# Optimization experiments

Measured on AMD Instinct MI355X. Metric: run time of the kernel, lower is better.

Reference implementation:

```python
import jax, jax.numpy as jnp
import numpy as np

N = 4096
D_IN = 512
D_H = 128
HEADS = 4
NEG_BIG = 1e10  # matches tf mask constant
LEAKY_ALPHA = 0.2  # tf.nn.leaky_relu default


def setup_inputs() -> dict:
    key = jax.random.key(0)
    ks = jax.random.split(key, 6)
    # 0/1 dense adjacency (faithful to tf.sparse.add producing dense 0/1 + mask)
    adjacency = jax.random.randint(ks[0], (N, N), 0, 2).astype(jnp.float32)
    # guarantee no empty rows (softmax over all -1e10 is degenerate)
    adjacency = adjacency.at[jnp.arange(N), jnp.arange(N)].set(1.0)
    input_feature = jax.random.normal(ks[1], (N, D_IN), dtype=jnp.float32)
    scale = 1.0 / np.sqrt(D_IN)
    kernels = jax.random.normal(ks[2], (HEADS, D_IN, D_H), dtype=jnp.float32) * scale
    biases = jnp.zeros((HEADS, D_H), dtype=jnp.float32)
    a_scale = 1.0 / np.sqrt(D_H)
    attn_self = jax.random.normal(ks[3], (HEADS, D_H), dtype=jnp.float32) * a_scale
    attn_neigh = jax.random.normal(ks[4], (HEADS, D_H), dtype=jnp.float32) * a_scale
    return {
        "adjacency": adjacency,
        "input_feature": input_feature,
        "kernels": kernels,
        "biases": biases,
        "attn_self": attn_self,
        "attn_neigh": attn_neigh,
    }


def reference(adjacency, input_feature, kernels, biases, attn_self, attn_neigh):
    # per-head feature projection: [H, N, D_h]
    feats = jnp.einsum("nd,hde->hne", input_feature, kernels)
    # additive attention logits
    a_s = jnp.einsum("hne,he->hn", feats, attn_self)   # [H, N]
    a_n = jnp.einsum("hne,he->hn", feats, attn_neigh)  # [H, N]
    dense = a_s[:, :, None] + a_n[:, None, :]          # [H, N, N]
    dense = jax.nn.leaky_relu(dense, negative_slope=LEAKY_ALPHA)
    mask = NEG_BIG * (adjacency - 1.0)                 # 0 where edge, -1e10 elsewhere
    dense = jax.nn.softmax(dense + mask[None, :, :], axis=-1)
    out = jnp.einsum("hnm,hme->hne", dense, feats) + biases[:, None, :]  # [H, N, D_h]
    # concat heads: [N, H*D_h]
    return jnp.transpose(out, (1, 0, 2)).reshape(out.shape[1], -1)
```

## Files before the change

kernel.cpp:

```cpp
#include <hip/hip_runtime.h>

#define NN 4096
#define DIN 512
#define DH 128
#define NH 4
#define L2E 1.44269504f

typedef float f32x4 __attribute__((ext_vector_type(4)));
typedef _Float16 f16x8 __attribute__((ext_vector_type(8)));
typedef _Float16 f16x4 __attribute__((ext_vector_type(4)));

__device__ __forceinline__ float leaky(float x){ return x > 0.f ? x : 0.2f*x; }

__global__ __launch_bounds__(256) void k_pack(
    const float* __restrict__ adj, unsigned int* __restrict__ bmg)
{
  int tId = blockIdx.x*256 + threadIdx.x;
  const float* p = adj + (size_t)tId*32;
  unsigned int b = 0;
  #pragma unroll
  for (int k=0;k<8;k++){
    f32x4 v = *(const f32x4*)(p + k*4);
    #pragma unroll
    for (int q=0;q<4;q++) b |= (v[q] > 0.5f) ? (1u << (k*4+q)) : 0u;
  }
  bmg[tId] = b;
}

__global__ __launch_bounds__(256) void k_gemm1(
    const float* __restrict__ X, const float* __restrict__ Kw,
    const float* __restrict__ attn_s, const float* __restrict__ attn_n,
    _Float16* __restrict__ featsT, float* __restrict__ a_s, float* __restrict__ a_n)
{
  const int it = blockIdx.x, h = blockIdx.y;
  const int i0 = it*64;
  const int t = threadIdx.x, w = t>>6, lane = t&63;
  const int eoff = (w>>1)*64, ioff = (w&1)*32;
  const int lg = lane>>4, li = lane&15;

  __shared__ _Float16 KT[128][40];
  __shared__ _Float16 XT[64][40];
  __shared__ float red_s[2][2][2][16];
  __shared__ float red_n[2][2][2][16];

  f32x4 acc[4][2] = {};

  for (int ks=0; ks<16; ++ks){
    const int d0 = ks*32;
    __syncthreads();
    #pragma unroll
    for (int q=0;q<4;q++){
      int f = t + 256*q;
      int e = f & 127, dg = (f>>7)*4;
      f16x4 hv;
      #pragma unroll
      for (int k=0;k<4;k++)
        hv[k] = (_Float16)Kw[(h*DIN + d0 + dg + k)*DH + e];
      *(f16x4*)&KT[e][dg] = hv;
    }
    #pragma unroll
    for (int q=0;q<2;q++){
      int f = t + 256*q;
      int i = f>>3, s = (f&7)*4;
      f32x4 v = *(const f32x4*)&X[(i0+i)*DIN + d0 + s];
      f16x4 hv; hv[0]=(_Float16)v[0]; hv[1]=(_Float16)v[1];
      hv[2]=(_Float16)v[2]; hv[3]=(_Float16)v[3];
      *(f16x4*)&XT[i][s] = hv;
    }
    __syncthreads();
    f16x8 af[4], bf[2];
    #pragma unroll
    for (int ef=0; ef<4; ++ef) af[ef] = *(const f16x8*)&KT[eoff + ef*16 + li][lg*8];
    #pragma unroll
    for (int f2=0; f2<2; ++f2) bf[f2] = *(const f16x8*)&XT[ioff + f2*16 + li][lg*8];
    #pragma unroll
    for (int ef=0; ef<4; ++ef)
      #pragma unroll
      for (int f2=0; f2<2; ++f2)
        acc[ef][f2] = __builtin_amdgcn_mfma_f32_16x16x32_f16(af[ef], bf[f2], acc[ef][f2], 0,0,0);
  }

  float ps[2] = {0,0}, pn[2] = {0,0};
  #pragma unroll
  for (int ef=0; ef<4; ++ef){
    #pragma unroll
    for (int r=0;r<4;r++){
      int e = eoff + ef*16 + lg*4 + r;
      float as_e = attn_s[h*DH + e];
      float an_e = attn_n[h*DH + e];
      #pragma unroll
      for (int f2=0; f2<2; ++f2){
        int irow = i0 + ioff + f2*16 + li;
        float v = acc[ef][f2][r];
        featsT[(h*DH + e)*NN + irow] = (_Float16)v;
        ps[f2] += v*as_e; pn[f2] += v*an_e;
      }
    }
  }
  #pragma unroll
  for (int f2=0; f2<2; ++f2){
    ps[f2] += __shfl_xor(ps[f2], 16); ps[f2] += __shfl_xor(ps[f2], 32);
    pn[f2] += __shfl_xor(pn[f2], 16); pn[f2] += __shfl_xor(pn[f2], 32);
  }
  if (lane < 16){
    red_s[w>>1][w&1][0][lane] = ps[0]; red_s[w>>1][w&1][1][lane] = ps[1];
    red_n[w>>1][w&1][0][lane] = pn[0]; red_n[w>>1][w&1][1][lane] = pn[1];
  }
  __syncthreads();
  if (t < 64){
    int ih = t>>5, fb = (t>>4)&1, l2 = t&15;
    a_s[h*NN + i0 + t] = red_s[0][ih][fb][l2] + red_s[1][ih][fb][l2];
    a_n[h*NN + i0 + t] = red_n[0][ih][fb][l2] + red_n[1][ih][fb][l2];
  }
}

__global__ void k_amax(const float* __restrict__ a_n, float* __restrict__ Amax,
                       float* __restrict__ EA_g, float* __restrict__ GA_g){
  int h = blockIdx.x, t = threadIdx.x;
  float m = -3.4e38f;
  for (int i=t; i<NN; i+=256){
    float v = a_n[h*NN+i];
    m = fmaxf(m, v);
    EA_g[h*NN+i] = __builtin_exp2f(v*L2E);
    GA_g[h*NN+i] = __builtin_exp2f(0.2f*v*L2E);
  }
  #pragma unroll
  for (int s=1; s<64; s<<=1) m = fmaxf(m, __shfl_xor(m, s));
  __shared__ float sm[4];
  if ((t&63)==0) sm[t>>6] = m;
  __syncthreads();
  if (t==0) Amax[h] = fmaxf(fmaxf(sm[0],sm[1]), fmaxf(sm[2],sm[3]));
}

__global__ __launch_bounds__(256, 3) void k_pv(
    const unsigned int* __restrict__ bmg, const _Float16* __restrict__ featsT,
    const float* __restrict__ a_s, const float* __restrict__ Amax,
    const float* __restrict__ EA_g, const float* __restrict__ GA_g,
    _Float16* __restrict__ Opart, float* __restrict__ Dpart)
{
  const int it = blockIdx.x, h = blockIdx.y, jcI = blockIdx.z;
  const int i0 = it*128, j0 = jcI*1024;
  const int t = threadIdx.x, w = t>>6, lane = t&63;
  const int lg = lane>>4, li = lane&15;

  __shared__ _Float16 ft[3][128*32];
  __shared__ float EA_s[1024], GA_s[1024];
  __shared__ unsigned char bm_s[128*144];

  __builtin_amdgcn_global_load_lds(
      (const __attribute__((address_space(1))) void*)(EA_g + h*NN + j0 + t*4),
      (__attribute__((address_space(3))) void*)(&EA_s[t*4]), 16, 0, 0);
  __builtin_amdgcn_global_load_lds(
      (const __attribute__((address_space(1))) void*)(GA_g + h*NN + j0 + t*4),
      (__attribute__((address_space(3))) void*)(&GA_s[t*4]), 16, 0, 0);
  #pragma unroll
  for (int p=0;p<4;p++){
    int idx = p*256 + t;
    int r = idx>>3, c = idx&7;
    uint4 v = *(const uint4*)((const char*)bmg + (size_t)(i0+r)*(NN/8) + jcI*128 + c*16);
    *(uint4*)&bm_s[r*144 + c*16] = v;
  }

  const int r0 = w*32 + li, r1 = r0 + 16;
  const float am = Amax[h];
  const float as0 = a_s[h*NN + i0 + r0];
  const float as1 = a_s[h*NN + i0 + r1];
  const float m0 = leaky(as0 + am), m1 = leaky(as1 + am);
  const float E0 = __builtin_exp2f((as0 - m0)*L2E);
  const float G0 = __builtin_exp2f((0.2f*as0 - m0)*L2E);
  const float E1 = __builtin_exp2f((as1 - m1)*L2E);
  const float G1 = __builtin_exp2f((0.2f*as1 - m1)*L2E);

  auto STAGE = [&](int buf, int js){
    #pragma unroll
    for (int q=0;q<2;q++){
      int idx = q*256 + t;
      int r = idx>>2, p = idx&3;
      int l = p ^ ((r>>1)&3);
      __builtin_amdgcn_global_load_lds(
          (const __attribute__((address_space(1))) void*)(featsT + (size_t)(h*DH + r)*NN + j0 + js*32 + l*8),
          (__attribute__((address_space(3))) void*)(&ft[buf][idx*8]), 16, 0, 0);
    }
  };

  STAGE(0, 0);
  STAGE(1, 1);
  __syncthreads();

  f32x4 acc0[8] = {}, acc1[8] = {};
  f32x4 accd0 = {}, accd1 = {};
  f16x8 ones;
  #pragma unroll
  for (int q=0;q<8;q++) ones[q] = (_Float16)1.0f;

  const int slot = lg ^ ((li>>1)&3);

  for (int js=0; js<32; ++js){
    const int cur = js % 3;
    asm volatile("s_waitcnt vmcnt(2)" ::: "memory");
    __builtin_amdgcn_s_barrier();
    {
      int nst = js+2 <= 31 ? js+2 : 31;
      STAGE((js+2) % 3, nst);
    }

    const int jb = js*32 + lg*8;
    f32x4 ea0 = *(const f32x4*)&EA_s[jb];
    f32x4 ea1 = *(const f32x4*)&EA_s[jb+4];
    f32x4 ga0 = *(const f32x4*)&GA_s[jb];
    f32x4 ga1 = *(const f32x4*)&GA_s[jb+4];
    unsigned int b0 = bm_s[r0*144 + js*4 + lg];
    unsigned int b1 = bm_s[r1*144 + js*4 + lg];

    f16x8 af0, af1;
    #pragma unroll
    for (int q=0;q<8;q++){
      float ev = (q<4) ? ea0[q] : ea1[q-4];
      float gv = (q<4) ? ga0[q] : ga1[q-4];
      float w0 = fmaxf(E0*ev, G0*gv);
      float w1 = fmaxf(E1*ev, G1*gv);
      unsigned mq0 = (unsigned)(((int)(b0 << (31-q))) >> 31);
      unsigned mq1 = (unsigned)(((int)(b1 << (31-q))) >> 31);
      w0 = __builtin_bit_cast(float, __builtin_bit_cast(unsigned, w0) & mq0);
      w1 = __builtin_bit_cast(float, __builtin_bit_cast(unsigned, w1) & mq1);
      af0[q] = (_Float16)w0;
      af1[q] = (_Float16)w1;
    }

    #pragma unroll
    for (int ef=0; ef<8; ++ef){
      f16x8 bfr = *(const f16x8*)&ft[cur][(ef*16+li)*32 + slot*8];
      acc0[ef] = __builtin_amdgcn_mfma_f32_16x16x32_f16(af0, bfr, acc0[ef], 0,0,0);
      acc1[ef] = __builtin_amdgcn_mfma_f32_16x16x32_f16(af1, bfr, acc1[ef], 0,0,0);
    }
    accd0 = __builtin_amdgcn_mfma_f32_16x16x32_f16(af0, ones, accd0, 0,0,0);
    accd1 = __builtin_amdgcn_mfma_f32_16x16x32_f16(af1, ones, accd1, 0,0,0);
  }

  const size_t chb = (size_t)(jcI*4 + h)*NN;
  if (li == 0){
    *(f32x4*)&Dpart[chb + i0 + w*32 + lg*4] = accd0;
    *(f32x4*)&Dpart[chb + i0 + w*32 + 16 + lg*4] = accd1;
  }
  #pragma unroll
  for (int ef=0; ef<8; ++ef)
    #pragma unroll
    for (int r=0;r<4;r++){
      int row0 = i0 + w*32 + lg*4 + r;
      Opart[(chb + row0)*DH + ef*16 + li] = (_Float16)acc0[ef][r];
      Opart[(chb + row0 + 16)*DH + ef*16 + li] = (_Float16)acc1[ef][r];
    }
}

__global__ __launch_bounds__(256) void k_out(
    const _Float16* __restrict__ Opart, const float* __restrict__ Dpart,
    const float* __restrict__ bias, float* __restrict__ out)
{
  int gid = blockIdx.x*256 + threadIdx.x;
  int base = gid*4;
  int i = base >> 9;
  int he = base & 511;
  int h = he >> 7;
  int e = he & 127;
  float n0=0,n1=0,n2=0,n3=0, den=0;
  #pragma unroll
  for (int jc=0; jc<4; ++jc){
    int ch = (jc*4+h)*NN + i;
    f16x4 v = *(const f16x4*)(Opart + (size_t)ch*DH + e);
    n0 += (float)v[0]; n1 += (float)v[1]; n2 += (float)v[2]; n3 += (float)v[3];
    den += Dpart[ch];
  }
  float inv = 1.f/den;
  f32x4 b4 = *(const f32x4*)&bias[he];
  f32x4 o; o[0]=n0*inv+b4[0]; o[1]=n1*inv+b4[1]; o[2]=n2*inv+b4[2]; o[3]=n3*inv+b4[3];
  *(f32x4*)&out[base] = o;
}

extern "C" void kernel_launch(void* const* d_in, const int* in_sizes, int n_in,
                              void* d_out, int out_size, void* d_ws, size_t ws_size,
                              hipStream_t stream)
{
  const float* adj   = (const float*)d_in[0];
  const float* X     = (const float*)d_in[1];
  const float* Kw    = (const float*)d_in[2];
  const float* bias  = (const float*)d_in[3];
  const float* atn_s = (const float*)d_in[4];
  const float* atn_n = (const float*)d_in[5];
  float* out = (float*)d_out;

  char* ws = (char*)d_ws;
  _Float16* featsT = (_Float16*)ws;
  unsigned int* bmg = (unsigned int*)(ws + ((size_t)4<<20));
  float* a_s  = (float*)(ws + (size_t)6*1024*1024);
  float* a_n  = a_s + NH*NN;
  float* Amax = a_n + NH*NN;
  float* EA_g = Amax + 64;
  float* GA_g = EA_g + NH*NN;
  float* Dpart = GA_g + NH*NN;
  _Float16* Opart = (_Float16*)(Dpart + 4*NH*NN);

  hipLaunchKernelGGL(k_pack, dim3(2048), dim3(256), 0, stream, adj, bmg);
  hipLaunchKernelGGL(k_gemm1, dim3(64,4), dim3(256), 0, stream,
                     X, Kw, atn_s, atn_n, featsT, a_s, a_n);
  hipLaunchKernelGGL(k_amax, dim3(4), dim3(256), 0, stream, a_n, Amax, EA_g, GA_g);
  hipLaunchKernelGGL(k_pv, dim3(32,4,4), dim3(256), 0, stream,
                     bmg, featsT, a_s, Amax, EA_g, GA_g, Opart, Dpart);
  hipLaunchKernelGGL(k_out, dim3(2048), dim3(256), 0, stream,
                     Opart, Dpart, bias, out);
}
```

Before: 73.55 us.

## Halve key chunk size for more PV blocks, coalesce adjacency packing

Shrinks the per-block key chunk in the attention-times-features kernel from 1024 to 512, doubling the grid to 1024 blocks and raising the occupancy hint to 4 blocks per CU. The goal is better load balance and latency hiding, at the cost of twice the partial-output traffic and reduction work in the final combine kernel. The adjacency packing kernel now reads coalesced float4 rows, builds nibbles in shared memory and merges them with bit tricks, instead of each thread striding across 32 floats. The PV inner loop also uses packed round-toward-zero f16 conversion and raises wave priority around the MFMA block.

```diff
diff --git a/kernel.cpp b/kernel.cpp
--- a/kernel.cpp
+++ b/kernel.cpp
@@ -4,27 +4,41 @@
 #define DIN 512
 #define DH 128
 #define NH 4
+#define JC 512
+#define NJC (NN/JC)
+#define JSTEPS (JC/32)
 #define L2E 1.44269504f
 
 typedef float f32x4 __attribute__((ext_vector_type(4)));
 typedef _Float16 f16x8 __attribute__((ext_vector_type(8)));
 typedef _Float16 f16x4 __attribute__((ext_vector_type(4)));
+typedef _Float16 f16x2 __attribute__((ext_vector_type(2)));
 
 __device__ __forceinline__ float leaky(float x){ return x > 0.f ? x : 0.2f*x; }
 
 __global__ __launch_bounds__(256) void k_pack(
     const float* __restrict__ adj, unsigned int* __restrict__ bmg)
 {
-  int tId = blockIdx.x*256 + threadIdx.x;
-  const float* p = adj + (size_t)tId*32;
-  unsigned int b = 0;
-  #pragma unroll
-  for (int k=0;k<8;k++){
-    f32x4 v = *(const f32x4*)(p + k*4);
-    #pragma unroll
-    for (int q=0;q<4;q++) b |= (v[q] > 0.5f) ? (1u << (k*4+q)) : 0u;
-  }
-  bmg[tId] = b;
+  __shared__ unsigned char nib[2][256];
+  const int t = threadIdx.x;
+  const size_t base = (size_t)blockIdx.x * 8192;
+  #pragma unroll
+  for (int it=0; it<8; ++it){
+    const size_t fb = base + it*1024;
+    f32x4 v = *(const f32x4*)&adj[fb + t*4];
+    unsigned nb = (v[0]>0.5f?1u:0u)|(v[1]>0.5f?2u:0u)|(v[2]>0.5f?4u:0u)|(v[3]>0.5f?8u:0u);
+    const int buf = it&1;
+    nib[buf][t] = (unsigned char)nb;
+    __syncthreads();
+    if (t < 32){
+      unsigned long long x = *(const unsigned long long*)&nib[buf][t*8];
+      x &= 0x0F0F0F0F0F0F0F0FULL;
+      x = (x | (x>>4))  & 0x00FF00FF00FF00FFULL;
+      x = (x | (x>>8))  & 0x0000FFFF0000FFFFULL;
+      x = (x | (x>>16));
+      bmg[fb/32 + t] = (unsigned int)x;
+    }
+  }
 }
 
 __global__ __launch_bounds__(256) void k_gemm1(
@@ -132,33 +146,36 @@
   if (t==0) Amax[h] = fmaxf(fmaxf(sm[0],sm[1]), fmaxf(sm[2],sm[3]));
 }
 
-__global__ __launch_bounds__(256, 3) void k_pv(
+__global__ __launch_bounds__(256, 4) void k_pv(
     const unsigned int* __restrict__ bmg, const _Float16* __restrict__ featsT,
     const float* __restrict__ a_s, const float* __restrict__ Amax,
     const float* __restrict__ EA_g, const float* __restrict__ GA_g,
     _Float16* __restrict__ Opart, float* __restrict__ Dpart)
 {
   const int it = blockIdx.x, h = blockIdx.y, jcI = blockIdx.z;
-  const int i0 = it*128, j0 = jcI*1024;
+  const int i0 = it*128, j0 = jcI*JC;
   const int t = threadIdx.x, w = t>>6, lane = t&63;
   const int lg = lane>>4, li = lane&15;
 
   __shared__ _Float16 ft[3][128*32];
-  __shared__ float EA_s[1024], GA_s[1024];
-  __shared__ unsigned char bm_s[128*144];
-
-  __builtin_amdgcn_global_load_lds(
-      (const __attribute__((address_space(1))) void*)(EA_g + h*NN + j0 + t*4),
-      (__attribute__((address_space(3))) void*)(&EA_s[t*4]), 16, 0, 0);
-  __builtin_amdgcn_global_load_lds(
-      (const __attribute__((address_space(1))) void*)(GA_g + h*NN + j0 + t*4),
-      (__attribute__((address_space(3))) void*)(&GA_s[t*4]), 16, 0, 0);
-  #pragma unroll
-  for (int p=0;p<4;p++){
+  __shared__ float EA_s[JC], GA_s[JC];
+  __shared__ unsigned char bm_s[128*80];
+
+  if (t < 128){
+    __builtin_amdgcn_global_load_lds(
+        (const __attribute__((address_space(1))) void*)(EA_g + h*NN + j0 + t*4),
+        (__attribute__((address_space(3))) void*)(&EA_s[t*4]), 16, 0, 0);
+  } else {
+    __builtin_amdgcn_global_load_lds(
+        (const __attribute__((address_space(1))) void*)(GA_g + h*NN + j0 + (t-128)*4),
+        (__attribute__((address_space(3))) void*)(&GA_s[(t-128)*4]), 16, 0, 0);
+  }
+  #pragma unroll
+  for (int p=0;p<2;p++){
     int idx = p*256 + t;
-    int r = idx>>3, c = idx&7;
-    uint4 v = *(const uint4*)((const char*)bmg + (size_t)(i0+r)*(NN/8) + jcI*128 + c*16);
-    *(uint4*)&bm_s[r*144 + c*16] = v;
+    int r = idx>>2, c = idx&3;
+    uint4 v = *(const uint4*)((const char*)bmg + (size_t)(i0+r)*(NN/8) + jcI*(JC/8) + c*16);
+    *(uint4*)&bm_s[r*80 + c*16] = v;
   }
 
   const int r0 = w*32 + li, r1 = r0 + 16;
@@ -195,12 +212,12 @@
 
   const int slot = lg ^ ((li>>1)&3);
 
-  for (int js=0; js<32; ++js){
+  for (int js=0; js<JSTEPS; ++js){
     const int cur = js % 3;
     asm volatile("s_waitcnt vmcnt(2)" ::: "memory");
     __builtin_amdgcn_s_barrier();
     {
-      int nst = js+2 <= 31 ? js+2 : 31;
+      int nst = js+2 <= JSTEPS-1 ? js+2 : JSTEPS-1;
       STAGE((js+2) % 3, nst);
     }
 
@@ -209,24 +226,28 @@
     f32x4 ea1 = *(const f32x4*)&EA_s[jb+4];
     f32x4 ga0 = *(const f32x4*)&GA_s[jb];
     f32x4 ga1 = *(const f32x4*)&GA_s[jb+4];
-    unsigned int b0 = bm_s[r0*144 + js*4 + lg];
-    unsigned int b1 = bm_s[r1*144 + js*4 + lg];
-
-    f16x8 af0, af1;
+    unsigned int b0 = bm_s[r0*80 + js*4 + lg];
+    unsigned int b1 = bm_s[r1*80 + js*4 + lg];
+
+    float wv0[8], wv1[8];
     #pragma unroll
     for (int q=0;q<8;q++){
       float ev = (q<4) ? ea0[q] : ea1[q-4];
       float gv = (q<4) ? ga0[q] : ga1[q-4];
       float w0 = fmaxf(E0*ev, G0*gv);
       float w1 = fmaxf(E1*ev, G1*gv);
-      unsigned mq0 = (unsigned)(((int)(b0 << (31-q))) >> 31);
-      unsigned mq1 = (unsigned)(((int)(b1 << (31-q))) >> 31);
-      w0 = __builtin_bit_cast(float, __builtin_bit_cast(unsigned, w0) & mq0);
-      w1 = __builtin_bit_cast(float, __builtin_bit_cast(unsigned, w1) & mq1);
-      af0[q] = (_Float16)w0;
-      af1[q] = (_Float16)w1;
-    }
-
+      wv0[q] = (b0 & (1u<<q)) ? w0 : 0.0f;
+      wv1[q] = (b1 & (1u<<q)) ? w1 : 0.0f;
+    }
+    union { f16x8 v; f16x2 h2[4]; } u0, u1;
+    #pragma unroll
+    for (int p=0;p<4;p++){
+      u0.h2[p] = __builtin_bit_cast(f16x2, __builtin_amdgcn_cvt_pkrtz(wv0[2*p], wv0[2*p+1]));
+      u1.h2[p] = __builtin_bit_cast(f16x2, __builtin_amdgcn_cvt_pkrtz(wv1[2*p], wv1[2*p+1]));
+    }
+    f16x8 af0 = u0.v, af1 = u1.v;
+
+    __builtin_amdgcn_s_setprio(1);
     #pragma unroll
     for (int ef=0; ef<8; ++ef){
       f16x8 bfr = *(const f16x8*)&ft[cur][(ef*16+li)*32 + slot*8];
@@ -235,6 +256,7 @@
     }
     accd0 = __builtin_amdgcn_mfma_f32_16x16x32_f16(af0, ones, accd0, 0,0,0);
     accd1 = __builtin_amdgcn_mfma_f32_16x16x32_f16(af1, ones, accd1, 0,0,0);
+    __builtin_amdgcn_s_setprio(0);
   }
 
   const size_t chb = (size_t)(jcI*4 + h)*NN;
@@ -264,7 +286,7 @@
   int e = he & 127;
   float n0=0,n1=0,n2=0,n3=0, den=0;
   #pragma unroll
-  for (int jc=0; jc<4; ++jc){
+  for (int jc=0; jc<NJC; ++jc){
     int ch = (jc*4+h)*NN + i;
     f16x4 v = *(const f16x4*)(Opart + (size_t)ch*DH + e);
     n0 += (float)v[0]; n1 += (float)v[1]; n2 += (float)v[2]; n3 += (float)v[3];
@@ -297,13 +319,13 @@
   float* EA_g = Amax + 64;
   float* GA_g = EA_g + NH*NN;
   float* Dpart = GA_g + NH*NN;
-  _Float16* Opart = (_Float16*)(Dpart + 4*NH*NN);
+  _Float16* Opart = (_Float16*)(Dpart + NJC*NH*NN);
 
   hipLaunchKernelGGL(k_pack, dim3(2048), dim3(256), 0, stream, adj, bmg);
   hipLaunchKernelGGL(k_gemm1, dim3(64,4), dim3(256), 0, stream,
                      X, Kw, atn_s, atn_n, featsT, a_s, a_n);
   hipLaunchKernelGGL(k_amax, dim3(4), dim3(256), 0, stream, a_n, Amax, EA_g, GA_g);
-  hipLaunchKernelGGL(k_pv, dim3(32,4,4), dim3(256), 0, stream,
+  hipLaunchKernelGGL(k_pv, dim3(32,4,NJC), dim3(256), 0, stream,
                      bmg, featsT, a_s, Amax, EA_g, GA_g, Opart, Dpart);
   hipLaunchKernelGGL(k_out, dim3(2048), dim3(256), 0, stream,
                      Opart, Dpart, bias, out);
```

Result: no change. 74.52 us (+1.3%).
